# Kernel optimization log

Measured on AMD Instinct MI355X. Metric: run time of the kernel, lower is better.

The kernel has to match this reference:

```python
import jax, jax.numpy as jnp
import numpy as np

B, T, S = 128, 256, 64
IN, H, K, CSL, OUT = 3, 512, 10, 60, 121


def setup_inputs() -> dict:
    key = jax.random.key(0)
    ks = jax.random.split(key, 10)
    s = lambda k, shape, sc: jax.random.normal(k, shape, jnp.float32) * sc
    return {
        "x": jax.random.normal(ks[0], (B, T, IN), jnp.float32),
        "sentences": jax.random.uniform(ks[1], (B, S, CSL), dtype=jnp.float32),
        "h1_h": jnp.zeros((B, H), jnp.float32),
        "h1_c": jnp.zeros((B, H), jnp.float32),
        "h2_h": jnp.zeros((B, H), jnp.float32),
        "h2_c": jnp.zeros((B, H), jnp.float32),
        # LSTMCell params (torch gate order i,f,g,o); b = b_ih + b_hh fused
        "W_ih_cell": s(ks[2], (4 * H, IN + CSL), 0.04),
        "W_hh_cell": s(ks[3], (4 * H, H), 0.04),
        "b_cell": jnp.zeros((4 * H,), jnp.float32),
        # second-layer nn.LSTM params
        "W_ih_l": s(ks[4], (4 * H, IN + CSL + H), 0.04),
        "W_hh_l": s(ks[5], (4 * H, H), 0.04),
        "b_l": jnp.zeros((4 * H,), jnp.float32),
        # fc1 -> window params, fc2 -> output
        "W1": s(ks[6], (3 * K, H), 0.04),
        "b1": jnp.zeros((3 * K,), jnp.float32),
        "W2": s(ks[7], (OUT, H), 0.04),
        "b2": jnp.zeros((OUT,), jnp.float32),
    }


def _lstm_step(h, c, xt, W_ih, W_hh, b):
    g = xt @ W_ih.T + h @ W_hh.T + b
    i, f, gg, o = jnp.split(g, 4, axis=-1)
    c2 = jax.nn.sigmoid(f) * c + jax.nn.sigmoid(i) * jnp.tanh(gg)
    h2 = jax.nn.sigmoid(o) * jnp.tanh(c2)
    return h2, c2


def reference(x, sentences, h1_h, h1_c, h2_h, h2_c,
              W_ih_cell, W_hh_cell, b_cell,
              W_ih_l, W_hh_l, b_l, W1, b1, W2, b2):
    u = jnp.arange(1, S + 1, dtype=x.dtype)[:, None]  # [S,1] char positions

    def step1(carry, xt):
        h, c, p = carry
        ip = jnp.exp(h @ W1.T + b1)                                     # [B,3K]
        # kappa part subtracts the previous step's kappa (quirk of the source)
        p_new = jnp.concatenate([ip[:, :2 * K], ip[:, 2 * K:] - p[:, 2 * K:]], axis=-1)
        a, be, ka = jnp.split(p_new[:, None, :], 3, axis=-1)            # each [B,1,K]
        phi = (a * jnp.exp(-be * (ka - u) ** 2)).sum(-1)                # [B,S]
        win = jnp.einsum('bs,bsc->bc', phi, sentences)                  # [B,CSL]
        h2, c2 = _lstm_step(h, c, jnp.concatenate([xt, win], axis=-1),
                            W_ih_cell, W_hh_cell, b_cell)
        return (h2, c2, p_new), (h2, win)

    xs = jnp.swapaxes(x, 0, 1)                                          # [T,B,IN]
    p0 = jnp.zeros((x.shape[0], 3 * K), x.dtype)
    (h1f, c1f, _), (hx, wins) = jax.lax.scan(step1, (h1_h, h1_c, p0), xs)

    feat = jnp.concatenate([xs, wins, hx], axis=-1)                     # [T,B,IN+CSL+H]

    def step2(carry, xt):
        h, c = carry
        h2, c2 = _lstm_step(h, c, xt, W_ih_l, W_hh_l, b_l)
        return (h2, c2), h2

    (h2f, c2f), ys = jax.lax.scan(step2, (h2_h, h2_c), feat)
    y = jnp.swapaxes(ys, 0, 1).reshape(-1, H)                           # [B*T,H]
    out = y @ W2.T + b2                                                 # [B*T,OUT]
    return out, h1f, c1f, h2f, c2f
```

## Files before the change

kernel.cpp:

```cpp
#include <hip/hip_runtime.h>
#include <hip/hip_bf16.h>
#include <math.h>

typedef __attribute__((ext_vector_type(8))) short short8;
typedef __attribute__((ext_vector_type(4))) float floatx4;

#define DEVFN static __device__ __forceinline__

constexpr int B = 128, T = 256, H = 512;
constexpr int OUTW = 121;
constexpr int SLOTW = 1664;
constexpr int LOOF  = 1088;
constexpr int SLOTE = B * SLOTW;
constexpr int NSLOT = T + 2;
constexpr int NG  = 2048;
constexpr int K1  = 576,  K1C = 18;
constexpr int K2  = 1088, K2C = 34;
constexpr int KW1P = 584, KW2P = 1096;

constexpr int O_WH1 = 0;
constexpr int O_WL1 = 37376;
constexpr int O_W1S = 74752;
constexpr int O_GSM = 137152;
constexpr int O_HS  = 137152;
constexpr int O_PP  = 139264;
constexpr int O_IPL = 145472;
constexpr int O_KL  = 145592;
constexpr int O_PHL = 145632;
constexpr int O_WAC = 145888;
constexpr int O_KPR = 146848;
constexpr int O_B1S = 146888;
constexpr int O_BIA = 147008;
constexpr int O_SENT = 147136;
constexpr int O_WH2 = 0;
constexpr int O_WL2 = 70144;
constexpr int O_GS2 = 140288;
constexpr int O_BI2 = 148608;
constexpr int LDS_SZ = 162496;

DEVFN __hip_bfloat16 bhi(float v) { return __float2bfloat16(v); }
DEVFN __hip_bfloat16 blo(float v, __hip_bfloat16 h) { return __float2bfloat16(v - __bfloat162float(h)); }
DEVFN float bf2f(__hip_bfloat16 h) { return __bfloat162float(h); }
DEVFN unsigned short bbits(__hip_bfloat16 h) { union { __hip_bfloat16 h; unsigned short u; } c; c.h = h; return c.u; }
DEVFN unsigned int pack2(float a, float b) {
  return (unsigned int)bbits(bhi(a)) | ((unsigned int)bbits(bhi(b)) << 16);
}
DEVFN void ast(unsigned int* p, unsigned int v) {
  __hip_atomic_store(p, v, __ATOMIC_RELAXED, __HIP_MEMORY_SCOPE_AGENT);
}
DEVFN int ald(int* p) {
  return __hip_atomic_load(p, __ATOMIC_RELAXED, __HIP_MEMORY_SCOPE_AGENT);
}

DEVFN void waitcnt8(int* base, int target) {
  if (threadIdx.x < 8) {
    int* p = base + threadIdx.x * 32;
    int g = 0;
    while (ald(p) < target && g < (1 << 24)) { ++g; __builtin_amdgcn_s_sleep(1); }
  }
  asm volatile("" ::: "memory");
  __syncthreads();
}
DEVFN void cnt_add(int* leaf) {
  asm volatile("s_waitcnt vmcnt(0)" ::: "memory");
  __syncthreads();
  if (threadIdx.x == 0)
    (void)__hip_atomic_fetch_add(leaf, 1, __ATOMIC_RELAXED, __HIP_MEMORY_SCOPE_AGENT);
}

__global__ __launch_bounds__(256) void k_pre(
    const float* __restrict__ x, const float* __restrict__ h1h, const float* __restrict__ h2h,
    const float* __restrict__ Wihc, const float* __restrict__ Whhc, const float* __restrict__ bc,
    const float* __restrict__ Wihl, const float* __restrict__ Whhl, const float* __restrict__ bl,
    const float* __restrict__ W2,
    __hip_bfloat16* __restrict__ fxHL,
    __hip_bfloat16* __restrict__ wc1, __hip_bfloat16* __restrict__ wc1l,
    __hip_bfloat16* __restrict__ wc2, __hip_bfloat16* __restrict__ wc2l,
    __hip_bfloat16* __restrict__ w2b, float* __restrict__ bi1, float* __restrict__ bi2,
    int* __restrict__ ctl)
{
  int idx = blockIdx.x * 256 + threadIdx.x;
  const int nwc1 = NG * K1, nwc2 = NG * K2, nw2b = 128 * 512, nbi = 2 * NG;
  const int nfh = B * H, nxj = T * B, nctl = 2048;
  if (idx < nwc1) {
    int n = idx / K1, col = idx - n * K1;
    int src = (n & 3) * H + (n >> 2);
    float v = (col < 63) ? Wihc[src * 63 + col]
            : (col == 63 ? 0.f : Whhc[src * 512 + (col - 64)]);
    __hip_bfloat16 h = bhi(v);
    wc1[n * K1 + col] = h; wc1l[n * K1 + col] = blo(v, h);
    return;
  }
  idx -= nwc1;
  if (idx < nwc2) {
    int n = idx / K2, col = idx - n * K2;
    int src = (n & 3) * H + (n >> 2);
    float v;
    if (col < 63)       v = Wihl[src * 575 + col];
    else if (col == 63) v = 0.f;
    else if (col < 576) v = Wihl[src * 575 + (col - 1)];
    else                v = Whhl[src * 512 + (col - 576)];
    __hip_bfloat16 h = bhi(v);
    wc2[n * K2 + col] = h; wc2l[n * K2 + col] = blo(v, h);
    return;
  }
  idx -= nwc2;
  if (idx < nw2b) {
    int n = idx >> 9, col = idx & 511;
    w2b[idx] = bhi(n < OUTW ? W2[n * 512 + col] : 0.f);
    return;
  }
  idx -= nw2b;
  if (idx < nbi) {
    int n = idx & (NG - 1);
    int src = (n & 3) * H + (n >> 2);
    if (idx < NG) bi1[n] = bc[src]; else bi2[n] = bl[src];
    return;
  }
  idx -= nbi;
  if (idx < nfh) {
    int b = idx >> 9, j = idx & 511;
    float v = h1h[idx];
    __hip_bfloat16 h = bhi(v);
    fxHL[b * SLOTW + 64 + j] = h;
    fxHL[b * SLOTW + LOOF + 64 + j] = blo(v, h);
    return;
  }
  idx -= nfh;
  if (idx < nfh) {
    int b = idx >> 9, j = idx & 511;
    fxHL[(size_t)SLOTE + b * SLOTW + 576 + j] = bhi(h2h[idx]);
    return;
  }
  idx -= nfh;
  if (idx < nxj) {
    int t = idx >> 7, b = idx & 127;
    float x0 = x[(b * T + t) * 3 + 0], x1 = x[(b * T + t) * 3 + 1];
    unsigned int* ph = (unsigned int*)(fxHL + (size_t)(t + 1) * SLOTE + b * SLOTW);
    ph[0] = pack2(x0, x1);
    unsigned int* pl = (unsigned int*)(fxHL + (size_t)(t + 1) * SLOTE + b * SLOTW + LOOF);
    pl[0] = 0u;
    return;
  }
  idx -= nxj;
  if (idx < nctl) ctl[idx] = 0;
}

template <int KWP>
DEVFN void gemm3(int tid, const __hip_bfloat16* __restrict__ Aslot, int m0,
                 const __hip_bfloat16* __restrict__ Wh, const __hip_bfloat16* __restrict__ Wl,
                 int cbeg, int cend, floatx4& a0, floatx4& a1)
{
  const int lane = tid & 63, wv = tid >> 6;
  const int lm = lane & 15, lk = (lane >> 4) << 3;
  const __hip_bfloat16* Ar = Aslot + (size_t)(m0 + wv * 16 + lm) * SLOTW;
  const __hip_bfloat16* W0h = Wh + lm * KWP;
  const __hip_bfloat16* W1h = Wh + (16 + lm) * KWP;
  const __hip_bfloat16* W0l = Wl + lm * KWP;
  const __hip_bfloat16* W1l = Wl + (16 + lm) * KWP;
  #pragma unroll 4
  for (int c = cbeg; c < cend; ++c) {
    int col = c * 32 + lk;
    short8 va  = *(const short8*)(Ar + col);
    short8 ua  = *(const short8*)(Ar + LOOF + col);
    short8 vb0 = *(const short8*)(W0h + col);
    short8 vb1 = *(const short8*)(W1h + col);
    short8 ub0 = *(const short8*)(W0l + col);
    short8 ub1 = *(const short8*)(W1l + col);
    a0 = __builtin_amdgcn_mfma_f32_16x16x32_bf16(va, vb0, a0, 0, 0, 0);
    a1 = __builtin_amdgcn_mfma_f32_16x16x32_bf16(va, vb1, a1, 0, 0, 0);
    a0 = __builtin_amdgcn_mfma_f32_16x16x32_bf16(va, ub0, a0, 0, 0, 0);
    a1 = __builtin_amdgcn_mfma_f32_16x16x32_bf16(va, ub1, a1, 0, 0, 0);
    a0 = __builtin_amdgcn_mfma_f32_16x16x32_bf16(ua, vb0, a0, 0, 0, 0);
    a1 = __builtin_amdgcn_mfma_f32_16x16x32_bf16(ua, vb1, a1, 0, 0, 0);
  }
}

DEVFN void store_gsm(int tid, float* Gsm, floatx4 a0, floatx4 a1) {
  const int lane = tid & 63, wv = tid >> 6;
  const int lm = lane & 15, rr = (lane >> 4) << 2;
  #pragma unroll
  for (int r = 0; r < 4; ++r) {
    Gsm[lm * 65 + wv * 16 + rr + r]        = a0[r];
    Gsm[(16 + lm) * 65 + wv * 16 + rr + r] = a1[r];
  }
}

__global__ __launch_bounds__(256, 1) void k_persist(
    __hip_bfloat16* __restrict__ fxHL,
    const __hip_bfloat16* __restrict__ wc1, const __hip_bfloat16* __restrict__ wc1l,
    const __hip_bfloat16* __restrict__ wc2, const __hip_bfloat16* __restrict__ wc2l,
    const float* __restrict__ bi1, const float* __restrict__ bi2,
    const float* __restrict__ c1init, const float* __restrict__ c2init,
    const float* __restrict__ xin, const float* __restrict__ sent,
    const float* __restrict__ W1, const float* __restrict__ b1,
    int* __restrict__ ctl,
    float* __restrict__ h1f, float* __restrict__ c1f,
    float* __restrict__ h2f, float* __restrict__ c2f)
{
  extern __shared__ char sm[];
  const int gid = blockIdx.x, tid = threadIdx.x;
  const int lane = tid & 63, wv = tid >> 6;
  const int lm = lane & 15, lk = (lane >> 4) << 3;

  if (gid < 128) {
    const int nt1 = gid >> 1, mh = gid & 1;
    const int n0 = nt1 * 32, m0 = mh * 64;
    const int brow = mh * 64 + nt1;
    const int leaf = (nt1 & 7) * 32;
    int* hcnt = ctl + mh * 256;
    int* wcnt = ctl + 512 + mh * 256;
    __hip_bfloat16* smWh = (__hip_bfloat16*)(sm + O_WH1);
    __hip_bfloat16* smWl = (__hip_bfloat16*)(sm + O_WL1);
    float* smW1 = (float*)(sm + O_W1S);
    float* Gsm  = (float*)(sm + O_GSM);
    float* hs   = (float*)(sm + O_HS);
    float* pp   = (float*)(sm + O_PP);
    float* ipl  = (float*)(sm + O_IPL);
    float* kl   = (float*)(sm + O_KL);
    float* phl  = (float*)(sm + O_PHL);
    float* wac  = (float*)(sm + O_WAC);
    float* kpr  = (float*)(sm + O_KPR);
    float* b1s  = (float*)(sm + O_B1S);
    float* bia  = (float*)(sm + O_BIA);
    float* ssent = (float*)(sm + O_SENT);

    for (int i = tid; i < 32 * 72; i += 256) {
      int r = i / 72, c8 = (i - r * 72) * 8;
      *(short8*)(smWh + r * KW1P + c8) = *(const short8*)(wc1  + (size_t)(n0 + r) * K1 + c8);
      *(short8*)(smWl + r * KW1P + c8) = *(const short8*)(wc1l + (size_t)(n0 + r) * K1 + c8);
    }
    for (int i = tid; i < 30 * 512; i += 256) {
      int j = i >> 9, c = i & 511;
      smW1[j * 520 + (c >> 6) * 65 + (c & 63)] = W1[i];
    }
    for (int i = tid; i < 64 * 60; i += 256)
      ssent[i] = sent[(size_t)brow * 64 * 60 + i];
    if (tid < 30) b1s[tid] = b1[tid];
    if (tid < 10) kpr[tid] = 0.f;
    if (tid < 32) bia[tid] = bi1[n0 + tid];
    __syncthreads();

    float creg[2];
    {
      int ml = tid >> 2, ppi = tid & 3;
      creg[0] = c1init[(m0 + ml) * H + nt1 * 8 + 2 * ppi + 0];
      creg[1] = c1init[(m0 + ml) * H + nt1 * 8 + 2 * ppi + 1];
    }

    const __hip_bfloat16* W0h = smWh + lm * KW1P;
    const __hip_bfloat16* W1h = smWh + (16 + lm) * KW1P;
    const __hip_bfloat16* W0l = smWl + lm * KW1P;
    const __hip_bfloat16* W1l = smWl + (16 + lm) * KW1P;

    for (int t = 0; t < T; ++t) {
      __hip_bfloat16* S1 = fxHL + (size_t)(t + 1) * SLOTE;
      __hip_bfloat16* S0 = fxHL + (size_t)t * SLOTE;

      waitcnt8(hcnt, 8 * t);

      const __hip_bfloat16* wrow = S0 + (size_t)brow * SLOTW;
      __hip_bfloat16 a0h = wrow[64 + tid];
      __hip_bfloat16 a0l = wrow[LOOF + 64 + tid];
      __hip_bfloat16 a1h = wrow[64 + 256 + tid];
      __hip_bfloat16 a1l = wrow[LOOF + 64 + 256 + tid];
      float x2v = xin[(brow * T + t) * 3 + 2];
      const __hip_bfloat16* Ar = S0 + (size_t)(m0 + wv * 16 + lm) * SLOTW;
      short8 pva[16], pua[16];
      if (wv != 0) {
        #pragma unroll
        for (int c = 0; c < 16; ++c) {
          pva[c] = *(const short8*)(Ar + (c + 2) * 32 + lk);
          pua[c] = *(const short8*)(Ar + LOOF + (c + 2) * 32 + lk);
        }
      }
      hs[(tid >> 6) * 66 + (tid & 63)] = bf2f(a0h) + bf2f(a0l);
      hs[((tid + 256) >> 6) * 66 + (tid & 63)] = bf2f(a1h) + bf2f(a1l);
      __syncthreads();

      if (tid < 240) {
        int j = tid >> 3, p = tid & 7;
        const float* wp = smW1 + j * 520 + p * 65;
        const float* hv = hs + p * 66;
        float s = 0.f;
        #pragma unroll 8
        for (int k = 0; k < 64; ++k) s += hv[k] * wp[k];
        pp[tid] = s;
      }
      __syncthreads();
      if (tid < 30) {
        float s = b1s[tid];
        #pragma unroll
        for (int p = 0; p < 8; ++p) s += pp[tid * 8 + p];
        float e = expf(s);
        ipl[tid] = e;
        if (tid >= 20) {
          float kap = e - kpr[tid - 20];
          kpr[tid - 20] = kap; kl[tid - 20] = kap;
        }
      }
      asm volatile("s_waitcnt lgkmcnt(0)" ::: "memory");
      if (tid < 64) {
        float u = (float)(tid + 1);
        float acc = 0.f;
        #pragma unroll
        for (int k = 0; k < 10; ++k) {
          float d = kl[k] - u;
          acc += ipl[k] * expf(-ipl[10 + k] * d * d);
        }
        phl[tid] = acc;
      }
      __syncthreads();
      if (tid < 240) {
        int c = tid >> 2, p = tid & 3;
        float acc = 0.f;
        #pragma unroll
        for (int s0 = 0; s0 < 16; ++s0)
          acc += phl[p * 16 + s0] * ssent[(p * 16 + s0) * 60 + c];
        wac[tid] = acc;
      }
      __syncthreads();
      if (tid < 31) {
        int d = 1 + tid;
        int c0 = 2 * d, c1 = 2 * d + 1;
        float v0, v1;
        if (c0 == 2) v0 = x2v;
        else { int j = (c0 - 3) * 4; v0 = wac[j] + wac[j + 1] + wac[j + 2] + wac[j + 3]; }
        if (c1 == 63) v1 = 0.f;
        else { int j = (c1 - 3) * 4; v1 = wac[j] + wac[j + 1] + wac[j + 2] + wac[j + 3]; }
        __hip_bfloat16 h0 = bhi(v0), h1v = bhi(v1);
        unsigned int* prow = (unsigned int*)(S1 + (size_t)brow * SLOTW);
        ast(prow + d, (unsigned int)bbits(h0) | ((unsigned int)bbits(h1v) << 16));
        ast(prow + (LOOF >> 1) + d,
            (unsigned int)bbits(blo(v0, h0)) | ((unsigned int)bbits(blo(v1, h1v)) << 16));
      }
      if (wv == 0) {
        asm volatile("s_waitcnt vmcnt(0)" ::: "memory");
        if (tid == 0)
          (void)__hip_atomic_fetch_add(wcnt + leaf, 1, __ATOMIC_RELAXED,
                                       __HIP_MEMORY_SCOPE_AGENT);
        #pragma unroll
        for (int c = 0; c < 16; ++c) {
          pva[c] = *(const short8*)(Ar + (c + 2) * 32 + lk);
          pua[c] = *(const short8*)(Ar + LOOF + (c + 2) * 32 + lk);
        }
      }

      floatx4 a0 = {0.f, 0.f, 0.f, 0.f}, a1 = a0;
      #pragma unroll
      for (int c = 0; c < 16; ++c) {
        int col = (c + 2) * 32 + lk;
        short8 vb0 = *(const short8*)(W0h + col);
        short8 vb1 = *(const short8*)(W1h + col);
        short8 ub0 = *(const short8*)(W0l + col);
        short8 ub1 = *(const short8*)(W1l + col);
        a0 = __builtin_amdgcn_mfma_f32_16x16x32_bf16(pva[c], vb0, a0, 0, 0, 0);
        a1 = __builtin_amdgcn_mfma_f32_16x16x32_bf16(pva[c], vb1, a1, 0, 0, 0);
        a0 = __builtin_amdgcn_mfma_f32_16x16x32_bf16(pva[c], ub0, a0, 0, 0, 0);
        a1 = __builtin_amdgcn_mfma_f32_16x16x32_bf16(pva[c], ub1, a1, 0, 0, 0);
        a0 = __builtin_amdgcn_mfma_f32_16x16x32_bf16(pua[c], vb0, a0, 0, 0, 0);
        a1 = __builtin_amdgcn_mfma_f32_16x16x32_bf16(pua[c], vb1, a1, 0, 0, 0);
      }
      waitcnt8(wcnt, 8 * (t + 1));
      gemm3<KW1P>(tid, S1, m0, smWh, smWl, 0, 2, a0, a1);
      store_gsm(tid, Gsm, a0, a1);
      __syncthreads();

      {
        int ml = tid >> 2, ppi = tid & 3;
        float v[2];
        #pragma unroll
        for (int j = 0; j < 2; ++j) {
          int nl = ppi * 8 + j * 4;
          float gi = Gsm[(nl + 0) * 65 + ml] + bia[nl + 0];
          float gf = Gsm[(nl + 1) * 65 + ml] + bia[nl + 1];
          float gg = Gsm[(nl + 2) * 65 + ml] + bia[nl + 2];
          float go = Gsm[(nl + 3) * 65 + ml] + bia[nl + 3];
          float ig = 1.f / (1.f + expf(-gi));
          float fg = 1.f / (1.f + expf(-gf));
          float gt = tanhf(gg);
          float og = 1.f / (1.f + expf(-go));
          float cn = fg * creg[j] + ig * gt;
          v[j] = og * tanhf(cn);
          creg[j] = cn;
        }
        __hip_bfloat16 h0 = bhi(v[0]), h1v = bhi(v[1]);
        unsigned int* prow = (unsigned int*)(S1 + (size_t)(m0 + ml) * SLOTW);
        int dw = 32 + nt1 * 4 + ppi;
        ast(prow + dw, (unsigned int)bbits(h0) | ((unsigned int)bbits(h1v) << 16));
        ast(prow + (LOOF >> 1) + dw,
            (unsigned int)bbits(blo(v[0], h0)) | ((unsigned int)bbits(blo(v[1], h1v)) << 16));
        if (t == T - 1) {
          int hg = nt1 * 8 + 2 * ppi;
          h1f[(m0 + ml) * H + hg]     = v[0];  c1f[(m0 + ml) * H + hg]     = creg[0];
          h1f[(m0 + ml) * H + hg + 1] = v[1];  c1f[(m0 + ml) * H + hg + 1] = creg[1];
        }
      }
      cnt_add(hcnt + leaf);
    }
  } else {
    const int g = gid - 128;
    const int nt2 = g >> 1, mh = g & 1;
    const int n0 = nt2 * 32, m0 = mh * 64;
    const int leaf = (nt2 & 7) * 32;
    int* hcnt = ctl + mh * 256;
    int* h2g  = ctl + 1024 + mh * 256;
    __hip_bfloat16* smWh = (__hip_bfloat16*)(sm + O_WH2);
    __hip_bfloat16* smWl = (__hip_bfloat16*)(sm + O_WL2);
    float* Gsm = (float*)(sm + O_GS2);
    float* bia = (float*)(sm + O_BI2);

    for (int i = tid; i < 32 * 136; i += 256) {
      int r = i / 136, c8 = (i - r * 136) * 8;
      *(short8*)(smWh + r * KW2P + c8) = *(const short8*)(wc2  + (size_t)(n0 + r) * K2 + c8);
      *(short8*)(smWl + r * KW2P + c8) = *(const short8*)(wc2l + (size_t)(n0 + r) * K2 + c8);
    }
    if (tid < 32) bia[tid] = bi2[n0 + tid];
    __syncthreads();

    float creg[2];
    {
      int ml = tid >> 2, ppi = tid & 3;
      creg[0] = c2init[(m0 + ml) * H + nt2 * 8 + 2 * ppi + 0];
      creg[1] = c2init[(m0 + ml) * H + nt2 * 8 + 2 * ppi + 1];
    }

    const __hip_bfloat16* W0h = smWh + lm * KW2P;
    const __hip_bfloat16* W1h = smWh + (16 + lm) * KW2P;
    const __hip_bfloat16* W0l = smWl + lm * KW2P;
    const __hip_bfloat16* W1l = smWl + (16 + lm) * KW2P;

    for (int t = 0; t < T; ++t) {
      __hip_bfloat16* S1 = fxHL + (size_t)(t + 1) * SLOTE;
      __hip_bfloat16* S2 = fxHL + (size_t)(t + 2) * SLOTE;
      const __hip_bfloat16* Ar = S1 + (size_t)(m0 + wv * 16 + lm) * SLOTW;

      waitcnt8(h2g, 8 * t);
      short8 pv2[16];
      #pragma unroll
      for (int c = 0; c < 16; ++c)
        pv2[c] = *(const short8*)(Ar + (K1C + c) * 32 + lk);
      floatx4 a0 = {0.f, 0.f, 0.f, 0.f}, a1 = a0;
      #pragma unroll
      for (int c = 0; c < 16; ++c) {
        int col = (K1C + c) * 32 + lk;
        short8 vb0 = *(const short8*)(W0h + col);
        short8 vb1 = *(const short8*)(W1h + col);
        short8 ub0 = *(const short8*)(W0l + col);
        short8 ub1 = *(const short8*)(W1l + col);
        a0 = __builtin_amdgcn_mfma_f32_16x16x32_bf16(pv2[c], vb0, a0, 0, 0, 0);
        a1 = __builtin_amdgcn_mfma_f32_16x16x32_bf16(pv2[c], vb1, a1, 0, 0, 0);
        a0 = __builtin_amdgcn_mfma_f32_16x16x32_bf16(pv2[c], ub0, a0, 0, 0, 0);
        a1 = __builtin_amdgcn_mfma_f32_16x16x32_bf16(pv2[c], ub1, a1, 0, 0, 0);
      }
      waitcnt8(hcnt, 8 * (t + 1));
      short8 qv[18], qu[18];
      #pragma unroll
      for (int c = 0; c < 18; ++c) {
        qv[c] = *(const short8*)(Ar + c * 32 + lk);
        qu[c] = *(const short8*)(Ar + LOOF + c * 32 + lk);
      }
      #pragma unroll
      for (int c = 0; c < 18; ++c) {
        int col = c * 32 + lk;
        short8 vb0 = *(const short8*)(W0h + col);
        short8 vb1 = *(const short8*)(W1h + col);
        short8 ub0 = *(const short8*)(W0l + col);
        short8 ub1 = *(const short8*)(W1l + col);
        a0 = __builtin_amdgcn_mfma_f32_16x16x32_bf16(qv[c], vb0, a0, 0, 0, 0);
        a1 = __builtin_amdgcn_mfma_f32_16x16x32_bf16(qv[c], vb1, a1, 0, 0, 0);
        a0 = __builtin_amdgcn_mfma_f32_16x16x32_bf16(qv[c], ub0, a0, 0, 0, 0);
        a1 = __builtin_amdgcn_mfma_f32_16x16x32_bf16(qv[c], ub1, a1, 0, 0, 0);
        a0 = __builtin_amdgcn_mfma_f32_16x16x32_bf16(qu[c], vb0, a0, 0, 0, 0);
        a1 = __builtin_amdgcn_mfma_f32_16x16x32_bf16(qu[c], vb1, a1, 0, 0, 0);
      }
      store_gsm(tid, Gsm, a0, a1);
      __syncthreads();

      {
        int ml = tid >> 2, ppi = tid & 3;
        float v[2];
        #pragma unroll
        for (int j = 0; j < 2; ++j) {
          int nl = ppi * 8 + j * 4;
          float gi = Gsm[(nl + 0) * 65 + ml] + bia[nl + 0];
          float gf = Gsm[(nl + 1) * 65 + ml] + bia[nl + 1];
          float gg = Gsm[(nl + 2) * 65 + ml] + bia[nl + 2];
          float go = Gsm[(nl + 3) * 65 + ml] + bia[nl + 3];
          float ig = 1.f / (1.f + expf(-gi));
          float fg = 1.f / (1.f + expf(-gf));
          float gt = tanhf(gg);
          float og = 1.f / (1.f + expf(-go));
          float cn = fg * creg[j] + ig * gt;
          v[j] = og * tanhf(cn);
          creg[j] = cn;
        }
        __hip_bfloat16 h0 = bhi(v[0]), h1v = bhi(v[1]);
        unsigned int* prow = (unsigned int*)(S2 + (size_t)(m0 + ml) * SLOTW);
        int dw = 288 + nt2 * 4 + ppi;
        ast(prow + dw, (unsigned int)bbits(h0) | ((unsigned int)bbits(h1v) << 16));
        if (t == T - 1) {
          int hg = nt2 * 8 + 2 * ppi;
          h2f[(m0 + ml) * H + hg]     = v[0];  c2f[(m0 + ml) * H + hg]     = creg[0];
          h2f[(m0 + ml) * H + hg + 1] = v[1];  c2f[(m0 + ml) * H + hg + 1] = creg[1];
        }
      }
      cnt_add(h2g + leaf);
    }
  }
}

__global__ __launch_bounds__(256) void k_out(
    const __hip_bfloat16* __restrict__ fxHL, const __hip_bfloat16* __restrict__ w2b,
    const float* __restrict__ b2, float* __restrict__ dout)
{
  int bid = blockIdx.x, tid = threadIdx.x;
  int mblk = bid >> 1, nblk = bid & 1;
  int wv = tid >> 6, lane = tid & 63;
  int lm = lane & 15, lk = (lane >> 4) << 3;
  int m0 = mblk * 128 + wv * 32;
  int n0 = nblk * 64;
  int r0 = m0 + lm, r1 = m0 + 16 + lm;
  const __hip_bfloat16* a0p = fxHL + (size_t)((r0 & 255) + 2) * SLOTE + (r0 >> 8) * SLOTW + 576;
  const __hip_bfloat16* a1p = fxHL + (size_t)((r1 & 255) + 2) * SLOTE + (r1 >> 8) * SLOTW + 576;
  floatx4 zz = {0.f, 0.f, 0.f, 0.f};
  floatx4 acc[2][4];
  #pragma unroll
  for (int mt = 0; mt < 2; ++mt)
    #pragma unroll
    for (int nt = 0; nt < 4; ++nt) acc[mt][nt] = zz;
  #pragma unroll
  for (int c = 0; c < 16; ++c) {
    int col = c * 32 + lk;
    short8 va0 = *(const short8*)(a0p + col);
    short8 va1 = *(const short8*)(a1p + col);
    short8 vb[4];
    #pragma unroll
    for (int nt = 0; nt < 4; ++nt)
      vb[nt] = *(const short8*)(w2b + (size_t)(n0 + nt * 16 + lm) * 512 + col);
    #pragma unroll
    for (int nt = 0; nt < 4; ++nt) {
      acc[0][nt] = __builtin_amdgcn_mfma_f32_16x16x32_bf16(va0, vb[nt], acc[0][nt], 0, 0, 0);
      acc[1][nt] = __builtin_amdgcn_mfma_f32_16x16x32_bf16(va1, vb[nt], acc[1][nt], 0, 0, 0);
    }
  }
  int rr = (lane >> 4) << 2;
  #pragma unroll
  for (int mt = 0; mt < 2; ++mt)
    #pragma unroll
    for (int nt = 0; nt < 4; ++nt)
      #pragma unroll
      for (int r = 0; r < 4; ++r) {
        int m = m0 + mt * 16 + rr + r;
        int n = n0 + nt * 16 + lm;
        if (n < OUTW) dout[(size_t)m * OUTW + n] = acc[mt][nt][r] + b2[n];
      }
}

extern "C" void kernel_launch(void* const* d_in, const int* in_sizes, int n_in,
                              void* d_out, int out_size, void* d_ws, size_t ws_size,
                              hipStream_t stream)
{
  (void)in_sizes; (void)n_in; (void)out_size; (void)ws_size;
  const float* x    = (const float*)d_in[0];
  const float* sent = (const float*)d_in[1];
  const float* h1h  = (const float*)d_in[2];
  const float* h1c  = (const float*)d_in[3];
  const float* h2h  = (const float*)d_in[4];
  const float* h2c  = (const float*)d_in[5];
  const float* Wihc = (const float*)d_in[6];
  const float* Whhc = (const float*)d_in[7];
  const float* bc   = (const float*)d_in[8];
  const float* Wihl = (const float*)d_in[9];
  const float* Whhl = (const float*)d_in[10];
  const float* bl   = (const float*)d_in[11];
  const float* W1   = (const float*)d_in[12];
  const float* b1   = (const float*)d_in[13];
  const float* W2   = (const float*)d_in[14];
  const float* b2   = (const float*)d_in[15];

  float* out = (float*)d_out;
  float* h1f = out + (size_t)B * T * OUTW;
  float* c1f = h1f + (size_t)B * H;
  float* h2f = c1f + (size_t)B * H;
  float* c2f = h2f + (size_t)B * H;

  char* p = (char*)d_ws;
  auto carve = [&](size_t bytes) { char* r = p; p += (bytes + 255) & ~(size_t)255; return r; };
  __hip_bfloat16* fxHL = (__hip_bfloat16*)carve((size_t)NSLOT * SLOTE * 2);
  __hip_bfloat16* wc1  = (__hip_bfloat16*)carve((size_t)NG * K1 * 2);
  __hip_bfloat16* wc1l = (__hip_bfloat16*)carve((size_t)NG * K1 * 2);
  __hip_bfloat16* wc2  = (__hip_bfloat16*)carve((size_t)NG * K2 * 2);
  __hip_bfloat16* wc2l = (__hip_bfloat16*)carve((size_t)NG * K2 * 2);
  __hip_bfloat16* w2b  = (__hip_bfloat16*)carve((size_t)128 * 512 * 2);
  float* bi1 = (float*)carve((size_t)NG * 4);
  float* bi2 = (float*)carve((size_t)NG * 4);
  int*   ctl = (int*)carve((size_t)2048 * 4);

  static bool attr_set = false;
  if (!attr_set) {
    (void)hipFuncSetAttribute((const void*)k_persist,
                              hipFuncAttributeMaxDynamicSharedMemorySize, LDS_SZ);
    attr_set = true;
  }

  k_pre<<<14232, 256, 0, stream>>>(x, h1h, h2h, Wihc, Whhc, bc, Wihl, Whhl, bl, W2,
                                   fxHL, wc1, wc1l, wc2, wc2l, w2b, bi1, bi2, ctl);
  k_persist<<<256, 256, LDS_SZ, stream>>>(fxHL, wc1, wc1l, wc2, wc2l, bi1, bi2,
                                          h1c, h2c, x, sent, W1, b1, ctl,
                                          h1f, c1f, h2f, c2f);
  k_out<<<512, 256, 0, stream>>>(fxHL, w2b, b2, out);
}
```

Measured before the change: 2.670 ms.

## Replace atomic counter barriers with per-wave flag stores and distributed polling

Inter-block synchronization in the persistent LSTM kernel previously used atomic fetch-add on 8 leaf counters, each followed by a block-wide barrier. It now uses per-wave (or per-block) monotonic flag stores, each on its own padded slot, and all 256 threads poll individual flags. The window-ready wait is narrowed to 16 lanes per wave without a trailing __syncthreads. The aim is to remove atomic contention and the block barriers before signalling. In exchange there are more flags to poll and a larger control area, and the weaker ordering carries some risk around memory visibility. The h-vector load for the window computation is also moved onto a single wave using vectorized short8 loads.

Result: slower. 3.376 ms (+26.4%).

```diff
diff --git a/kernel.cpp b/kernel.cpp
--- a/kernel.cpp
+++ b/kernel.cpp
@@ -17,6 +17,11 @@
 constexpr int K1  = 576,  K1C = 18;
 constexpr int K2  = 1088, K2C = 34;
 constexpr int KW1P = 584, KW2P = 1096;
+
+constexpr int O_HFL  = 0;
+constexpr int O_WFL  = 16384;
+constexpr int O_H2FL = 20480;
+constexpr int NCTL   = 36864;
 
 constexpr int O_WH1 = 0;
 constexpr int O_WL1 = 37376;
@@ -51,21 +56,18 @@
 DEVFN int ald(int* p) {
   return __hip_atomic_load(p, __ATOMIC_RELAXED, __HIP_MEMORY_SCOPE_AGENT);
 }
-
-DEVFN void waitcnt8(int* base, int target) {
-  if (threadIdx.x < 8) {
+DEVFN void fst(int* p, int v) {
+  __hip_atomic_store(p, v, __ATOMIC_RELAXED, __HIP_MEMORY_SCOPE_AGENT);
+}
+
+DEVFN void wait256(int* base, int target) {
+  {
     int* p = base + threadIdx.x * 32;
     int g = 0;
     while (ald(p) < target && g < (1 << 24)) { ++g; __builtin_amdgcn_s_sleep(1); }
   }
   asm volatile("" ::: "memory");
   __syncthreads();
-}
-DEVFN void cnt_add(int* leaf) {
-  asm volatile("s_waitcnt vmcnt(0)" ::: "memory");
-  __syncthreads();
-  if (threadIdx.x == 0)
-    (void)__hip_atomic_fetch_add(leaf, 1, __ATOMIC_RELAXED, __HIP_MEMORY_SCOPE_AGENT);
 }
 
 __global__ __launch_bounds__(256) void k_pre(
@@ -81,7 +83,7 @@
 {
   int idx = blockIdx.x * 256 + threadIdx.x;
   const int nwc1 = NG * K1, nwc2 = NG * K2, nw2b = 128 * 512, nbi = 2 * NG;
-  const int nfh = B * H, nxj = T * B, nctl = 2048;
+  const int nfh = B * H, nxj = T * B, nctl = NCTL;
   if (idx < nwc1) {
     int n = idx / K1, col = idx - n * K1;
     int src = (n & 3) * H + (n >> 2);
@@ -207,9 +209,8 @@
     const int nt1 = gid >> 1, mh = gid & 1;
     const int n0 = nt1 * 32, m0 = mh * 64;
     const int brow = mh * 64 + nt1;
-    const int leaf = (nt1 & 7) * 32;
-    int* hcnt = ctl + mh * 256;
-    int* wcnt = ctl + 512 + mh * 256;
+    int* hfl = ctl + O_HFL + mh * 8192;
+    int* wfl = ctl + O_WFL + mh * 2048;
     __hip_bfloat16* smWh = (__hip_bfloat16*)(sm + O_WH1);
     __hip_bfloat16* smWl = (__hip_bfloat16*)(sm + O_WL1);
     float* smW1 = (float*)(sm + O_W1S);
@@ -257,14 +258,16 @@
       __hip_bfloat16* S1 = fxHL + (size_t)(t + 1) * SLOTE;
       __hip_bfloat16* S0 = fxHL + (size_t)t * SLOTE;
 
-      waitcnt8(hcnt, 8 * t);
+      wait256(hfl, t);
 
       const __hip_bfloat16* wrow = S0 + (size_t)brow * SLOTW;
-      __hip_bfloat16 a0h = wrow[64 + tid];
-      __hip_bfloat16 a0l = wrow[LOOF + 64 + tid];
-      __hip_bfloat16 a1h = wrow[64 + 256 + tid];
-      __hip_bfloat16 a1l = wrow[LOOF + 64 + 256 + tid];
-      float x2v = xin[(brow * T + t) * 3 + 2];
+      float x2v = 0.f;
+      short8 wrh, wrl;
+      if (wv == 0) {
+        wrh = *(const short8*)(wrow + 64 + lane * 8);
+        wrl = *(const short8*)(wrow + LOOF + 64 + lane * 8);
+        x2v = xin[(brow * T + t) * 3 + 2];
+      }
       const __hip_bfloat16* Ar = S0 + (size_t)(m0 + wv * 16 + lm) * SLOTW;
       short8 pva[16], pua[16];
       if (wv != 0) {
@@ -274,8 +277,13 @@
           pua[c] = *(const short8*)(Ar + LOOF + (c + 2) * 32 + lk);
         }
       }
-      hs[(tid >> 6) * 66 + (tid & 63)] = bf2f(a0h) + bf2f(a0l);
-      hs[((tid + 256) >> 6) * 66 + (tid & 63)] = bf2f(a1h) + bf2f(a1l);
+      if (wv == 0) {
+        float* hd = hs + (lane >> 3) * 66 + (lane & 7) * 8;
+        #pragma unroll
+        for (int j = 0; j < 8; ++j)
+          hd[j] = bf2f(((const __hip_bfloat16*)&wrh)[j]) +
+                  bf2f(((const __hip_bfloat16*)&wrl)[j]);
+      }
       __syncthreads();
 
       if (tid < 240) {
@@ -336,9 +344,7 @@
       }
       if (wv == 0) {
         asm volatile("s_waitcnt vmcnt(0)" ::: "memory");
-        if (tid == 0)
-          (void)__hip_atomic_fetch_add(wcnt + leaf, 1, __ATOMIC_RELAXED,
-                                       __HIP_MEMORY_SCOPE_AGENT);
+        if (tid == 0) fst(wfl + nt1 * 32, t + 1);
         #pragma unroll
         for (int c = 0; c < 16; ++c) {
           pva[c] = *(const short8*)(Ar + (c + 2) * 32 + lk);
@@ -361,7 +367,12 @@
         a0 = __builtin_amdgcn_mfma_f32_16x16x32_bf16(pua[c], vb0, a0, 0, 0, 0);
         a1 = __builtin_amdgcn_mfma_f32_16x16x32_bf16(pua[c], vb1, a1, 0, 0, 0);
       }
-      waitcnt8(wcnt, 8 * (t + 1));
+      if (lane < 16) {
+        int* p = wfl + (wv * 16 + lane) * 32;
+        int g = 0;
+        while (ald(p) < t + 1 && g < (1 << 24)) { ++g; __builtin_amdgcn_s_sleep(1); }
+      }
+      asm volatile("" ::: "memory");
       gemm3<KW1P>(tid, S1, m0, smWh, smWl, 0, 2, a0, a1);
       store_gsm(tid, Gsm, a0, a1);
       __syncthreads();
@@ -396,15 +407,15 @@
           h1f[(m0 + ml) * H + hg + 1] = v[1];  c1f[(m0 + ml) * H + hg + 1] = creg[1];
         }
       }
-      cnt_add(hcnt + leaf);
+      asm volatile("s_waitcnt vmcnt(0)" ::: "memory");
+      if (lane == 0) fst(hfl + (nt1 * 4 + wv) * 32, t + 1);
     }
   } else {
     const int g = gid - 128;
     const int nt2 = g >> 1, mh = g & 1;
     const int n0 = nt2 * 32, m0 = mh * 64;
-    const int leaf = (nt2 & 7) * 32;
-    int* hcnt = ctl + mh * 256;
-    int* h2g  = ctl + 1024 + mh * 256;
+    int* hfl  = ctl + O_HFL + mh * 8192;
+    int* h2fl = ctl + O_H2FL + mh * 8192;
     __hip_bfloat16* smWh = (__hip_bfloat16*)(sm + O_WH2);
     __hip_bfloat16* smWl = (__hip_bfloat16*)(sm + O_WL2);
     float* Gsm = (float*)(sm + O_GS2);
@@ -435,7 +446,7 @@
       __hip_bfloat16* S2 = fxHL + (size_t)(t + 2) * SLOTE;
       const __hip_bfloat16* Ar = S1 + (size_t)(m0 + wv * 16 + lm) * SLOTW;
 
-      waitcnt8(h2g, 8 * t);
+      wait256(h2fl, t);
       short8 pv2[16];
       #pragma unroll
       for (int c = 0; c < 16; ++c)
@@ -453,7 +464,7 @@
         a0 = __builtin_amdgcn_mfma_f32_16x16x32_bf16(pv2[c], ub0, a0, 0, 0, 0);
         a1 = __builtin_amdgcn_mfma_f32_16x16x32_bf16(pv2[c], ub1, a1, 0, 0, 0);
       }
-      waitcnt8(hcnt, 8 * (t + 1));
+      wait256(hfl, t + 1);
       short8 qv[18], qu[18];
       #pragma unroll
       for (int c = 0; c < 18; ++c) {
@@ -505,7 +516,8 @@
           h2f[(m0 + ml) * H + hg + 1] = v[1];  c2f[(m0 + ml) * H + hg + 1] = creg[1];
         }
       }
-      cnt_add(h2g + leaf);
+      asm volatile("s_waitcnt vmcnt(0)" ::: "memory");
+      if (lane == 0) fst(h2fl + (nt2 * 4 + wv) * 32, t + 1);
     }
   }
 }
@@ -595,7 +607,7 @@
   __hip_bfloat16* w2b  = (__hip_bfloat16*)carve((size_t)128 * 512 * 2);
   float* bi1 = (float*)carve((size_t)NG * 4);
   float* bi2 = (float*)carve((size_t)NG * 4);
-  int*   ctl = (int*)carve((size_t)2048 * 4);
+  int*   ctl = (int*)carve((size_t)NCTL * 4);
 
   static bool attr_set = false;
   if (!attr_set) {
@@ -604,7 +616,7 @@
     attr_set = true;
   }
 
-  k_pre<<<14232, 256, 0, stream>>>(x, h1h, h2h, Wihc, Whhc, bc, Wihl, Whhl, bl, W2,
+  k_pre<<<14368, 256, 0, stream>>>(x, h1h, h2h, Wihc, Whhc, bc, Wihl, Whhl, bl, W2,
                                    fxHL, wc1, wc1l, wc2, wc2l, w2b, bi1, bi2, ctl);
   k_persist<<<256, 256, LDS_SZ, stream>>>(fxHL, wc1, wc1l, wc2, wc2l, bi1, bi2,
                                           h1c, h2c, x, sent, W1, b1, ctl,
```

## Poll sentinel-filled hidden state instead of counter barrier for window computation

Applied to the files above, without the earlier changes.

Adds a prep kernel that fills the hidden-state slots with a sentinel bf16 pattern. In the persistent kernel, wave 0 spins on the slot data itself until no sentinel remains, then starts the window/attention computation before the counter-based barrier. This lets the fc1/window path begin as soon as its own row's data lands rather than waiting for all producers. The cost is an extra sentinel-fill kernel over all slots and a correctness risk if a real value matches the sentinel bit pattern (0x7FFF is a bf16 NaN).

After: 2.930 ms. 9.7% more time.

```diff
diff --git a/kernel.cpp b/kernel.cpp
--- a/kernel.cpp
+++ b/kernel.cpp
@@ -17,6 +17,7 @@
 constexpr int K1  = 576,  K1C = 18;
 constexpr int K2  = 1088, K2C = 34;
 constexpr int KW1P = 584, KW2P = 1096;
+constexpr unsigned int SENT = 0x7FFF7FFFu;
 
 constexpr int O_WH1 = 0;
 constexpr int O_WL1 = 37376;
@@ -41,6 +42,9 @@
 DEVFN __hip_bfloat16 bhi(float v) { return __float2bfloat16(v); }
 DEVFN __hip_bfloat16 blo(float v, __hip_bfloat16 h) { return __float2bfloat16(v - __bfloat162float(h)); }
 DEVFN float bf2f(__hip_bfloat16 h) { return __bfloat162float(h); }
+DEVFN float bfu(unsigned short u) {
+  union { unsigned short u; __hip_bfloat16 h; } c; c.u = u; return __bfloat162float(c.h);
+}
 DEVFN unsigned short bbits(__hip_bfloat16 h) { union { __hip_bfloat16 h; unsigned short u; } c; c.h = h; return c.u; }
 DEVFN unsigned int pack2(float a, float b) {
   return (unsigned int)bbits(bhi(a)) | ((unsigned int)bbits(bhi(b)) << 16);
@@ -50,6 +54,9 @@
 }
 DEVFN int ald(int* p) {
   return __hip_atomic_load(p, __ATOMIC_RELAXED, __HIP_MEMORY_SCOPE_AGENT);
+}
+DEVFN unsigned int uald(const unsigned int* p) {
+  return __hip_atomic_load((unsigned int*)p, __ATOMIC_RELAXED, __HIP_MEMORY_SCOPE_AGENT);
 }
 
 DEVFN void waitcnt8(int* base, int target) {
@@ -66,6 +73,16 @@
   __syncthreads();
   if (threadIdx.x == 0)
     (void)__hip_atomic_fetch_add(leaf, 1, __ATOMIC_RELAXED, __HIP_MEMORY_SCOPE_AGENT);
+}
+
+__global__ __launch_bounds__(256) void k_sent(__hip_bfloat16* __restrict__ fxHL)
+{
+  int blk = blockIdx.x;
+  int slot = (blk >> 7) + 1;
+  int row  = blk & 127;
+  unsigned int* rb = (unsigned int*)(fxHL + (size_t)slot * SLOTE + (size_t)row * SLOTW);
+  rb[32 + threadIdx.x] = SENT;
+  rb[(LOOF >> 1) + 32 + threadIdx.x] = SENT;
 }
 
 __global__ __launch_bounds__(256) void k_pre(
@@ -257,14 +274,45 @@
       __hip_bfloat16* S1 = fxHL + (size_t)(t + 1) * SLOTE;
       __hip_bfloat16* S0 = fxHL + (size_t)t * SLOTE;
 
+      __syncthreads();
+
+      float x2v = 0.f;
+      if (wv == 0) {
+        const unsigned int* rb = (const unsigned int*)(S0 + (size_t)brow * SLOTW);
+        const unsigned int* hp = rb + 32 + lane * 4;
+        const unsigned int* lp = rb + (LOOF >> 1) + 32 + lane * 4;
+        unsigned int dh[4], dl[4];
+        #pragma unroll
+        for (int q = 0; q < 4; ++q) { dh[q] = uald(hp + q); dl[q] = uald(lp + q); }
+        int g = 0;
+        for (;;) {
+          bool any = false;
+          #pragma unroll
+          for (int q = 0; q < 4; ++q) {
+            if (dh[q] == SENT) any = true;
+            if (dl[q] == SENT) any = true;
+          }
+          if (!any || g >= (1 << 24)) break;
+          __builtin_amdgcn_s_sleep(1); ++g;
+          #pragma unroll
+          for (int q = 0; q < 4; ++q) {
+            if (dh[q] == SENT) dh[q] = uald(hp + q);
+            if (dl[q] == SENT) dl[q] = uald(lp + q);
+          }
+        }
+        x2v = xin[(brow * T + t) * 3 + 2];
+        float* hd = hs + (lane >> 3) * 66 + (lane & 7) * 8;
+        #pragma unroll
+        for (int q = 0; q < 4; ++q) {
+          hd[2 * q]     = bfu((unsigned short)(dh[q] & 0xFFFFu)) +
+                          bfu((unsigned short)(dl[q] & 0xFFFFu));
+          hd[2 * q + 1] = bfu((unsigned short)(dh[q] >> 16)) +
+                          bfu((unsigned short)(dl[q] >> 16));
+        }
+      }
+
       waitcnt8(hcnt, 8 * t);
 
-      const __hip_bfloat16* wrow = S0 + (size_t)brow * SLOTW;
-      __hip_bfloat16 a0h = wrow[64 + tid];
-      __hip_bfloat16 a0l = wrow[LOOF + 64 + tid];
-      __hip_bfloat16 a1h = wrow[64 + 256 + tid];
-      __hip_bfloat16 a1l = wrow[LOOF + 64 + 256 + tid];
-      float x2v = xin[(brow * T + t) * 3 + 2];
       const __hip_bfloat16* Ar = S0 + (size_t)(m0 + wv * 16 + lm) * SLOTW;
       short8 pva[16], pua[16];
       if (wv != 0) {
@@ -274,9 +322,6 @@
           pua[c] = *(const short8*)(Ar + LOOF + (c + 2) * 32 + lk);
         }
       }
-      hs[(tid >> 6) * 66 + (tid & 63)] = bf2f(a0h) + bf2f(a0l);
-      hs[((tid + 256) >> 6) * 66 + (tid & 63)] = bf2f(a1h) + bf2f(a1l);
-      __syncthreads();
 
       if (tid < 240) {
         int j = tid >> 3, p = tid & 7;
@@ -604,6 +649,7 @@
     attr_set = true;
   }
 
+  k_sent<<<32768, 256, 0, stream>>>(fxHL);
   k_pre<<<14232, 256, 0, stream>>>(x, h1h, h2h, Wihc, Whhc, bc, Wihl, Whhl, bl, W2,
                                    fxHL, wc1, wc1l, wc2, wc2l, w2b, bi1, bi2, ctl);
   k_persist<<<256, 256, LDS_SZ, stream>>>(fxHL, wc1, wc1l, wc2, wc2l, bi1, bi2,
```
